# Performance work log

Hardware: AMD Instinct MI355X
Metric: run time of the kernel (lower is better)

Reference implementation:

```python
import math
import jax, jax.numpy as jnp
import numpy as np

B, S, D_MODEL, NUM_HEADS = 4, 2048, 1024, 16
D_N = D_MODEL // NUM_HEADS  # 64


def setup_inputs() -> dict:
    key = jax.random.key(0)
    ks = jax.random.split(key, 10)
    scale = 1.0 / math.sqrt(D_MODEL)
    return {
        "q": jax.random.normal(ks[0], (B, S, D_MODEL), dtype=jnp.float32),
        "k": jax.random.normal(ks[1], (B, S, D_MODEL), dtype=jnp.float32),
        "v": jax.random.normal(ks[2], (B, S, D_MODEL), dtype=jnp.float32),
        "mask": jax.random.uniform(ks[3], (B, S, S), dtype=jnp.float32),
        "w_q": jax.random.normal(ks[4], (D_N, D_MODEL), dtype=jnp.float32) * scale,
        "b_q": jnp.zeros((D_N,), dtype=jnp.float32),
        "w_k": jax.random.normal(ks[5], (D_N, D_MODEL), dtype=jnp.float32) * scale,
        "b_k": jnp.zeros((D_N,), dtype=jnp.float32),
        "w_v": jax.random.normal(ks[6], (D_N, D_MODEL), dtype=jnp.float32) * scale,
        "b_v": jnp.zeros((D_N,), dtype=jnp.float32),
    }


def reference(q, k, v, mask, w_q, b_q, w_k, b_k, w_v, b_v):
    # Linear projections d_model -> d_n (torch Linear: x @ W.T + b)
    qp = jnp.einsum("bsd,nd->bsn", q, w_q) + b_q  # [B,S,d_n]
    kp = jnp.einsum("bsd,nd->bsn", k, w_k) + b_k
    vp = jnp.einsum("bsd,nd->bsn", v, w_v) + b_v
    # Scaled dot-product scores with additive mask penalty
    scores = jnp.einsum("bqn,bkn->bqk", qp, kp) / math.sqrt(D_N) + mask * (-1e9)
    attn = jax.nn.softmax(scores, axis=-1)  # [B,S,S]
    return jnp.einsum("bqk,bkn->bqn", attn, vp)  # [B,S,d_n]
```

## Files before the change

### kernel.cpp

```cpp
#include <hip/hip_runtime.h>
#include <hip/hip_bf16.h>

#define BB 4
#define SS 2048
#define DM 1024
#define DN 64

typedef short short8 __attribute__((ext_vector_type(8)));
typedef float f32x4 __attribute__((ext_vector_type(4)));
typedef unsigned short ushort;

__device__ __forceinline__ ushort f2bf(float f) {
    union { float f; unsigned u; } v; v.f = f;
    unsigned r = v.u + 0x7fffu + ((v.u >> 16) & 1u);
    return (ushort)(r >> 16);
}

__global__ __launch_bounds__(256) void prep_w(
    const float* __restrict__ wq, const float* __restrict__ wk,
    const float* __restrict__ wv, ushort* __restrict__ w_bf)
{
    int i = blockIdx.x * 256 + threadIdx.x;
    int p = i >> 14;
    int j = (i & 16383) * 4;
    const float* src = (p == 0) ? wq : (p == 1) ? wk : wv;
    float4 f = *(const float4*)(src + j);
    ushort o[4] = { f2bf(f.x), f2bf(f.y), f2bf(f.z), f2bf(f.w) };
    *(unsigned long long*)(w_bf + p * 65536 + j) = *(unsigned long long*)o;
}

__global__ __launch_bounds__(128) void proj_kernel(
    const float* __restrict__ q, const float* __restrict__ k, const float* __restrict__ v,
    const ushort* __restrict__ w_bf,
    const float* __restrict__ bq, const float* __restrict__ bk, const float* __restrict__ bvp,
    ushort* __restrict__ qp, ushort* __restrict__ kp, ushort* __restrict__ vpT)
{
    const int tid  = threadIdx.x;
    const int proj = blockIdx.y;
    const int wv_id = tid >> 6;
    const int lane  = tid & 63;
    const int l16   = lane & 15;
    const int quad  = lane >> 4;
    const int g     = blockIdx.x * 2 + wv_id;
    const int m0    = g * 16;

    const float* x     = (proj == 0) ? q  : (proj == 1) ? k  : v;
    const ushort* wb   = w_bf + proj * 65536;
    const float* bias  = (proj == 0) ? bq : (proj == 1) ? bk : bvp;

    const float* arow = x + (size_t)(m0 + l16) * DM + quad * 8;

    f32x4 acc[4];
#pragma unroll
    for (int t = 0; t < 4; t++) acc[t] = (f32x4){0.f, 0.f, 0.f, 0.f};

#pragma unroll 2
    for (int kb = 0; kb < DM; kb += 32) {
        float4 f0 = *(const float4*)(arow + kb);
        float4 f1 = *(const float4*)(arow + kb + 4);
        ushort ta[8] = { f2bf(f0.x), f2bf(f0.y), f2bf(f0.z), f2bf(f0.w),
                         f2bf(f1.x), f2bf(f1.y), f2bf(f1.z), f2bf(f1.w) };
        short8 a = *(short8*)ta;
#pragma unroll
        for (int t = 0; t < 4; t++) {
            short8 b = *(const short8*)(wb + (size_t)(t * 16 + l16) * DM + kb + quad * 8);
            acc[t] = __builtin_amdgcn_mfma_f32_16x16x32_bf16(a, b, acc[t], 0, 0, 0);
        }
    }

#pragma unroll
    for (int t = 0; t < 4; t++) {
        int n = t * 16 + l16;
        float bb_ = bias[n];
#pragma unroll
        for (int r = 0; r < 4; r++) {
            int grow = m0 + quad * 4 + r;
            ushort h = f2bf(acc[t][r] + bb_);
            if (proj == 0)      qp[(size_t)grow * DN + n] = h;
            else if (proj == 1) kp[(size_t)grow * DN + n] = h;
            else {
                int bb = grow >> 11, s = grow & 2047;
                vpT[((size_t)bb * DN + n) * SS + s] = h;
            }
        }
    }
}

__global__ __launch_bounds__(256, 4) void flash_kernel(
    const float* __restrict__ mask,
    const ushort* __restrict__ qp,
    const ushort* __restrict__ kp,
    const ushort* __restrict__ vpT,
    float* __restrict__ part_O,
    float* __restrict__ part_ml,
    int nslice, int keys_per_slice)
{
    __shared__ __align__(16) ushort p_lds[4][16][80];

    const int tid  = threadIdx.x;
    const int wv   = tid >> 6;
    const int lane = tid & 63;
    const int l16  = lane & 15;
    const int quad = lane >> 4;

    const int gw     = blockIdx.x * 4 + wv;
    const int qg     = gw & 127;
    const int rest   = gw >> 7;
    const int slice  = rest % nslice;
    const int b      = rest / nslice;

    const ushort* qbase = qp + ((size_t)b * SS + qg * 16 + l16) * DN + quad * 8;
    short8 aq0 = *(const short8*)(qbase);
    short8 aq1 = *(const short8*)(qbase + 32);

    float m_r[4] = { -__builtin_inff(), -__builtin_inff(),
                     -__builtin_inff(), -__builtin_inff() };
    float l_r[4] = { 0.f, 0.f, 0.f, 0.f };
    f32x4 Oacc[4];
#pragma unroll
    for (int t = 0; t < 4; t++) Oacc[t] = (f32x4){0.f, 0.f, 0.f, 0.f};

    const size_t mrow0 = ((size_t)b * SS + qg * 16 + quad * 4) * SS;
    const int k_begin = slice * keys_per_slice;
    const int k_end   = k_begin + keys_per_slice;

    for (int k0 = k_begin; k0 < k_end; k0 += 64) {
        float mk[4][4];
#pragma unroll
        for (int t = 0; t < 4; t++)
#pragma unroll
            for (int r = 0; r < 4; r++)
                mk[t][r] = mask[mrow0 + (size_t)r * SS + k0 + t * 16 + l16];

        f32x4 sc[4];
#pragma unroll
        for (int t = 0; t < 4; t++) {
            const ushort* kb_ = kp + ((size_t)b * SS + k0 + t * 16 + l16) * DN + quad * 8;
            short8 bk0 = *(const short8*)(kb_);
            short8 bk1 = *(const short8*)(kb_ + 32);
            f32x4 z = (f32x4){0.f, 0.f, 0.f, 0.f};
            z = __builtin_amdgcn_mfma_f32_16x16x32_bf16(aq0, bk0, z, 0, 0, 0);
            z = __builtin_amdgcn_mfma_f32_16x16x32_bf16(aq1, bk1, z, 0, 0, 0);
            sc[t] = z;
        }

#pragma unroll
        for (int r = 0; r < 4; r++) {
            float s[4];
            float tmax = -__builtin_inff();
#pragma unroll
            for (int t = 0; t < 4; t++) {
                s[t] = sc[t][r] * 0.125f - 1e9f * mk[t][r];
                tmax = fmaxf(tmax, s[t]);
            }
#pragma unroll
            for (int off = 8; off >= 1; off >>= 1)
                tmax = fmaxf(tmax, __shfl_xor(tmax, off, 16));
            float mnew  = fmaxf(m_r[r], tmax);
            float alpha = __expf(m_r[r] - mnew);
            m_r[r] = mnew;
            float rs = 0.f;
#pragma unroll
            for (int t = 0; t < 4; t++) {
                float pv = __expf(s[t] - mnew);
                rs += pv;
                p_lds[wv][quad * 4 + r][t * 16 + l16] = f2bf(pv);
            }
#pragma unroll
            for (int off = 8; off >= 1; off >>= 1)
                rs += __shfl_xor(rs, off, 16);
            l_r[r] = l_r[r] * alpha + rs;
#pragma unroll
            for (int tf = 0; tf < 4; tf++)
                Oacc[tf][r] *= alpha;
        }

        short8 ap0 = *(const short8*)&p_lds[wv][l16][quad * 8];
        short8 ap1 = *(const short8*)&p_lds[wv][l16][32 + quad * 8];
#pragma unroll
        for (int tf = 0; tf < 4; tf++) {
            const ushort* vb_ = vpT + ((size_t)b * DN + tf * 16 + l16) * SS + k0 + quad * 8;
            short8 bv0 = *(const short8*)(vb_);
            short8 bv1 = *(const short8*)(vb_ + 32);
            Oacc[tf] = __builtin_amdgcn_mfma_f32_16x16x32_bf16(ap0, bv0, Oacc[tf], 0, 0, 0);
            Oacc[tf] = __builtin_amdgcn_mfma_f32_16x16x32_bf16(ap1, bv1, Oacc[tf], 0, 0, 0);
        }
    }

    const int rowg = (b * SS + qg * 16) + quad * 4;
#pragma unroll
    for (int r = 0; r < 4; r++) {
        size_t row = (size_t)rowg + r;
        if (l16 == 0) {
            part_ml[((size_t)slice * (BB * SS) + row) * 2 + 0] = m_r[r];
            part_ml[((size_t)slice * (BB * SS) + row) * 2 + 1] = l_r[r];
        }
#pragma unroll
        for (int tf = 0; tf < 4; tf++)
            part_O[((size_t)slice * (BB * SS) + row) * DN + tf * 16 + l16] = Oacc[tf][r];
    }
}

__global__ __launch_bounds__(256) void combine_kernel(
    const float* __restrict__ part_O, const float* __restrict__ part_ml,
    float* __restrict__ out, int nslice)
{
    const int tid = threadIdx.x;
    const int row = blockIdx.x * 4 + (tid >> 6);
    const int f   = tid & 63;

    float ms[8], ls[8];
    float M = -__builtin_inff();
    for (int i = 0; i < nslice; i++) {
        ms[i] = part_ml[((size_t)i * (BB * SS) + row) * 2 + 0];
        ls[i] = part_ml[((size_t)i * (BB * SS) + row) * 2 + 1];
        M = fmaxf(M, ms[i]);
    }
    float L = 0.f, acc = 0.f;
    for (int i = 0; i < nslice; i++) {
        float e = __expf(ms[i] - M);
        L += e * ls[i];
        acc += e * part_O[((size_t)i * (BB * SS) + row) * DN + f];
    }
    out[(size_t)row * DN + f] = acc / L;
}

extern "C" void kernel_launch(void* const* d_in, const int* in_sizes, int n_in,
                              void* d_out, int out_size, void* d_ws, size_t ws_size,
                              hipStream_t stream) {
    const float* q    = (const float*)d_in[0];
    const float* k    = (const float*)d_in[1];
    const float* v    = (const float*)d_in[2];
    const float* mask = (const float*)d_in[3];
    const float* wq   = (const float*)d_in[4];
    const float* bq   = (const float*)d_in[5];
    const float* wk   = (const float*)d_in[6];
    const float* bk   = (const float*)d_in[7];
    const float* wv   = (const float*)d_in[8];
    const float* bv   = (const float*)d_in[9];
    float* out = (float*)d_out;

    char* p = (char*)d_ws;
    ushort* w_bf = (ushort*)p;                 p += 3 * 65536 * sizeof(ushort);
    ushort* qp   = (ushort*)p;                 p += (size_t)BB * SS * DN * 2;
    ushort* kp   = (ushort*)p;                 p += (size_t)BB * SS * DN * 2;
    ushort* vpT  = (ushort*)p;                 p += (size_t)BB * SS * DN * 2;
    size_t fixed = (size_t)(p - (char*)d_ws);

    int split = 8;
    while (split > 1 &&
           fixed + (size_t)split * ((size_t)BB * SS * 2 * 4 + (size_t)BB * SS * DN * 4) > ws_size)
        split >>= 1;

    float* part_ml = (float*)p;                p += (size_t)split * BB * SS * 2 * 4;
    float* part_O  = (float*)p;

    int keys_per_slice = SS / split;

    prep_w<<<192, 256, 0, stream>>>(wq, wk, wv, w_bf);
    proj_kernel<<<dim3(256, 3), 128, 0, stream>>>(q, k, v, w_bf, bq, bk, bv, qp, kp, vpT);
    flash_kernel<<<128 * split, 256, 0, stream>>>(mask, qp, kp, vpT, part_O, part_ml,
                                                  split, keys_per_slice);
    combine_kernel<<<(BB * SS) / 4, 256, 0, stream>>>(part_O, part_ml, out, split);
}
```

Baseline: 226.6 us.

## Double-buffer K/mask loads, template slice size, store partials in bf16

The flash kernel is templated on keys-per-slice so the loop fully unrolls. It prefetches the next tile's K fragments and mask values into a second register buffer and issues the V loads before the score MFMAs, so memory latency overlaps with compute. Partial outputs are stored as bf16 to halve partial-output traffic, and the projection kernel's unroll factor and launch bounds are raised. The extra registers lower the occupancy bound from 4 to 2 blocks, and the bf16 partials add rounding error.

After: 240.1 us. 5.9% more time.

```diff
diff --git a/kernel.cpp b/kernel.cpp
--- a/kernel.cpp
+++ b/kernel.cpp
@@ -14,6 +14,9 @@
     union { float f; unsigned u; } v; v.f = f;
     unsigned r = v.u + 0x7fffu + ((v.u >> 16) & 1u);
     return (ushort)(r >> 16);
+}
+__device__ __forceinline__ float bf2f(ushort h) {
+    union { unsigned u; float f; } v; v.u = ((unsigned)h) << 16; return v.f;
 }
 
 __global__ __launch_bounds__(256) void prep_w(
@@ -29,7 +32,7 @@
     *(unsigned long long*)(w_bf + p * 65536 + j) = *(unsigned long long*)o;
 }
 
-__global__ __launch_bounds__(128) void proj_kernel(
+__global__ __launch_bounds__(128, 2) void proj_kernel(
     const float* __restrict__ q, const float* __restrict__ k, const float* __restrict__ v,
     const ushort* __restrict__ w_bf,
     const float* __restrict__ bq, const float* __restrict__ bk, const float* __restrict__ bvp,
@@ -54,7 +57,7 @@
 #pragma unroll
     for (int t = 0; t < 4; t++) acc[t] = (f32x4){0.f, 0.f, 0.f, 0.f};
 
-#pragma unroll 2
+#pragma unroll 4
     for (int kb = 0; kb < DM; kb += 32) {
         float4 f0 = *(const float4*)(arow + kb);
         float4 f1 = *(const float4*)(arow + kb + 4);
@@ -86,16 +89,19 @@
     }
 }
 
-__global__ __launch_bounds__(256, 4) void flash_kernel(
+template<int KPS>
+__global__ __launch_bounds__(256, 2) void flash_kernel(
     const float* __restrict__ mask,
     const ushort* __restrict__ qp,
     const ushort* __restrict__ kp,
     const ushort* __restrict__ vpT,
-    float* __restrict__ part_O,
-    float* __restrict__ part_ml,
-    int nslice, int keys_per_slice)
-{
-    __shared__ __align__(16) ushort p_lds[4][16][80];
+    ushort* __restrict__ part_O,
+    float* __restrict__ part_ml)
+{
+    constexpr int NSLICE = SS / KPS;
+    constexpr int NIT    = KPS / 64;
+
+    __shared__ __align__(16) ushort p_lds[4][16][72];
 
     const int tid  = threadIdx.x;
     const int wv   = tid >> 6;
@@ -103,11 +109,11 @@
     const int l16  = lane & 15;
     const int quad = lane >> 4;
 
-    const int gw     = blockIdx.x * 4 + wv;
-    const int qg     = gw & 127;
-    const int rest   = gw >> 7;
-    const int slice  = rest % nslice;
-    const int b      = rest / nslice;
+    const int gw    = blockIdx.x * 4 + wv;
+    const int qg    = gw & 127;
+    const int rest  = gw >> 7;
+    const int slice = rest % NSLICE;
+    const int b     = rest / NSLICE;
 
     const ushort* qbase = qp + ((size_t)b * SS + qg * 16 + l16) * DN + quad * 8;
     short8 aq0 = *(const short8*)(qbase);
@@ -121,26 +127,48 @@
     for (int t = 0; t < 4; t++) Oacc[t] = (f32x4){0.f, 0.f, 0.f, 0.f};
 
     const size_t mrow0 = ((size_t)b * SS + qg * 16 + quad * 4) * SS;
-    const int k_begin = slice * keys_per_slice;
-    const int k_end   = k_begin + keys_per_slice;
-
-    for (int k0 = k_begin; k0 < k_end; k0 += 64) {
-        float mk[4][4];
-#pragma unroll
-        for (int t = 0; t < 4; t++)
-#pragma unroll
-            for (int r = 0; r < 4; r++)
-                mk[t][r] = mask[mrow0 + (size_t)r * SS + k0 + t * 16 + l16];
-
-        f32x4 sc[4];
+    const int k_begin = slice * KPS;
+
+    float  mk[2][4][4];
+    short8 bk0[2][4], bk1[2][4];
+
+    auto load_tile = [&](int buf, int k0) {
 #pragma unroll
         for (int t = 0; t < 4; t++) {
             const ushort* kb_ = kp + ((size_t)b * SS + k0 + t * 16 + l16) * DN + quad * 8;
-            short8 bk0 = *(const short8*)(kb_);
-            short8 bk1 = *(const short8*)(kb_ + 32);
+            bk0[buf][t] = *(const short8*)(kb_);
+            bk1[buf][t] = *(const short8*)(kb_ + 32);
+        }
+#pragma unroll
+        for (int t = 0; t < 4; t++)
+#pragma unroll
+            for (int r = 0; r < 4; r++)
+                mk[buf][t][r] = mask[mrow0 + (size_t)r * SS + k0 + t * 16 + l16];
+    };
+
+    load_tile(0, k_begin);
+
+#pragma unroll
+    for (int it = 0; it < NIT; ++it) {
+        const int cur = it & 1;
+        const int k0  = k_begin + it * 64;
+
+        if (it + 1 < NIT) load_tile(cur ^ 1, k0 + 64);
+
+        short8 bv0[4], bv1[4];
+#pragma unroll
+        for (int tf = 0; tf < 4; tf++) {
+            const ushort* vb_ = vpT + ((size_t)b * DN + tf * 16 + l16) * SS + k0 + quad * 8;
+            bv0[tf] = *(const short8*)(vb_);
+            bv1[tf] = *(const short8*)(vb_ + 32);
+        }
+
+        f32x4 sc[4];
+#pragma unroll
+        for (int t = 0; t < 4; t++) {
             f32x4 z = (f32x4){0.f, 0.f, 0.f, 0.f};
-            z = __builtin_amdgcn_mfma_f32_16x16x32_bf16(aq0, bk0, z, 0, 0, 0);
-            z = __builtin_amdgcn_mfma_f32_16x16x32_bf16(aq1, bk1, z, 0, 0, 0);
+            z = __builtin_amdgcn_mfma_f32_16x16x32_bf16(aq0, bk0[cur][t], z, 0, 0, 0);
+            z = __builtin_amdgcn_mfma_f32_16x16x32_bf16(aq1, bk1[cur][t], z, 0, 0, 0);
             sc[t] = z;
         }
 
@@ -150,7 +178,7 @@
             float tmax = -__builtin_inff();
 #pragma unroll
             for (int t = 0; t < 4; t++) {
-                s[t] = sc[t][r] * 0.125f - 1e9f * mk[t][r];
+                s[t] = sc[t][r] * 0.125f - 1e9f * mk[cur][t][r];
                 tmax = fmaxf(tmax, s[t]);
             }
 #pragma unroll
@@ -179,11 +207,8 @@
         short8 ap1 = *(const short8*)&p_lds[wv][l16][32 + quad * 8];
 #pragma unroll
         for (int tf = 0; tf < 4; tf++) {
-            const ushort* vb_ = vpT + ((size_t)b * DN + tf * 16 + l16) * SS + k0 + quad * 8;
-            short8 bv0 = *(const short8*)(vb_);
-            short8 bv1 = *(const short8*)(vb_ + 32);
-            Oacc[tf] = __builtin_amdgcn_mfma_f32_16x16x32_bf16(ap0, bv0, Oacc[tf], 0, 0, 0);
-            Oacc[tf] = __builtin_amdgcn_mfma_f32_16x16x32_bf16(ap1, bv1, Oacc[tf], 0, 0, 0);
+            Oacc[tf] = __builtin_amdgcn_mfma_f32_16x16x32_bf16(ap0, bv0[tf], Oacc[tf], 0, 0, 0);
+            Oacc[tf] = __builtin_amdgcn_mfma_f32_16x16x32_bf16(ap1, bv1[tf], Oacc[tf], 0, 0, 0);
         }
     }
 
@@ -197,12 +222,13 @@
         }
 #pragma unroll
         for (int tf = 0; tf < 4; tf++)
-            part_O[((size_t)slice * (BB * SS) + row) * DN + tf * 16 + l16] = Oacc[tf][r];
+            part_O[((size_t)slice * (BB * SS) + row) * DN + tf * 16 + l16] =
+                f2bf(Oacc[tf][r]);
     }
 }
 
 __global__ __launch_bounds__(256) void combine_kernel(
-    const float* __restrict__ part_O, const float* __restrict__ part_ml,
+    const ushort* __restrict__ part_O, const float* __restrict__ part_ml,
     float* __restrict__ out, int nslice)
 {
     const int tid = threadIdx.x;
@@ -220,7 +246,7 @@
     for (int i = 0; i < nslice; i++) {
         float e = __expf(ms[i] - M);
         L += e * ls[i];
-        acc += e * part_O[((size_t)i * (BB * SS) + row) * DN + f];
+        acc += e * bf2f(part_O[((size_t)i * (BB * SS) + row) * DN + f]);
     }
     out[(size_t)row * DN + f] = acc / L;
 }
@@ -249,17 +275,19 @@
 
     int split = 8;
     while (split > 1 &&
-           fixed + (size_t)split * ((size_t)BB * SS * 2 * 4 + (size_t)BB * SS * DN * 4) > ws_size)
+           fixed + (size_t)split * ((size_t)BB * SS * 2 * 4 + (size_t)BB * SS * DN * 2) > ws_size)
         split >>= 1;
 
-    float* part_ml = (float*)p;                p += (size_t)split * BB * SS * 2 * 4;
-    float* part_O  = (float*)p;
-
-    int keys_per_slice = SS / split;
+    float*  part_ml = (float*)p;               p += (size_t)split * BB * SS * 2 * 4;
+    ushort* part_O  = (ushort*)p;
 
     prep_w<<<192, 256, 0, stream>>>(wq, wk, wv, w_bf);
     proj_kernel<<<dim3(256, 3), 128, 0, stream>>>(q, k, v, w_bf, bq, bk, bv, qp, kp, vpT);
-    flash_kernel<<<128 * split, 256, 0, stream>>>(mask, qp, kp, vpT, part_O, part_ml,
-                                                  split, keys_per_slice);
+    switch (split) {
+        case 8:  flash_kernel<256> <<<128 * 8, 256, 0, stream>>>(mask, qp, kp, vpT, part_O, part_ml); break;
+        case 4:  flash_kernel<512> <<<128 * 4, 256, 0, stream>>>(mask, qp, kp, vpT, part_O, part_ml); break;
+        case 2:  flash_kernel<1024><<<128 * 2, 256, 0, stream>>>(mask, qp, kp, vpT, part_O, part_ml); break;
+        default: flash_kernel<2048><<<128 * 1, 256, 0, stream>>>(mask, qp, kp, vpT, part_O, part_ml); break;
+    }
     combine_kernel<<<(BB * SS) / 4, 256, 0, stream>>>(part_O, part_ml, out, split);
 }
```
